# Kernel tuning notes

Measured on AMD Instinct MI355X. Metric: run time of the kernel, lower is better.

Reference implementation:

```python
import jax, jax.numpy as jnp
import numpy as np

D_MODEL = 1024
NUM_HEADS = 16
D_K = D_MODEL // NUM_HEADS


def setup_inputs() -> dict:
    key = jax.random.key(0)
    ks = jax.random.split(key, 11)
    B, S = 2, 2048
    scale = 1.0 / np.sqrt(D_MODEL)
    inp = {
        "v": jax.random.normal(ks[0], (B, S, D_MODEL), jnp.float32),
        "k": jax.random.normal(ks[1], (B, S, D_MODEL), jnp.float32),
        "q": jax.random.normal(ks[2], (B, S, D_MODEL), jnp.float32),
        "Wv": jax.random.normal(ks[3], (D_MODEL, D_MODEL), jnp.float32) * scale,
        "bv": jax.random.normal(ks[4], (D_MODEL,), jnp.float32) * 0.01,
        "Wk": jax.random.normal(ks[5], (D_MODEL, D_MODEL), jnp.float32) * scale,
        "bk": jax.random.normal(ks[6], (D_MODEL,), jnp.float32) * 0.01,
        "Wq": jax.random.normal(ks[7], (D_MODEL, D_MODEL), jnp.float32) * scale,
        "bq": jax.random.normal(ks[8], (D_MODEL,), jnp.float32) * 0.01,
        "Wo": jax.random.normal(ks[9], (D_MODEL, D_MODEL), jnp.float32) * scale,
        "bo": jax.random.normal(ks[10], (D_MODEL,), jnp.float32) * 0.01,
    }
    return inp


def reference(v, k, q, Wv, bv, Wk, bk, Wq, bq, Wo, bo):
    B, S, _ = q.shape
    # Linear projections (torch Linear: x @ W.T + b)
    vp = v @ Wv.T + bv
    kp = k @ Wk.T + bk
    qp = q @ Wq.T + bq
    # Split heads: [B, S, H, Dk]
    vp = vp.reshape(B, S, NUM_HEADS, D_K)
    kp = kp.reshape(B, S, NUM_HEADS, D_K)
    qp = qp.reshape(B, S, NUM_HEADS, D_K)
    # Scores [B, H, S, S], scaled softmax attention
    scores = jnp.einsum("bqhd,bkhd->bhqk", qp, kp) / jnp.sqrt(jnp.float32(D_K)).astype(qp.dtype)
    attn = jax.nn.softmax(scores, axis=-1)
    out = jnp.einsum("bhqk,bkhd->bqhd", attn, vp)
    out = out.reshape(B, S, D_MODEL)
    return out @ Wo.T + bo
```

## Files before the change

### kernel.cpp

```cpp
#include <hip/hip_runtime.h>
#include <math.h>

#define D 1024
#define NH 16
#define DK 64
#define S_LEN 2048
#define QSCALE 0.18033688011112f

using short8 = __attribute__((ext_vector_type(8))) short;
using f32x4  = __attribute__((ext_vector_type(4))) float;

#define MFMA16(a, b, c) __builtin_amdgcn_mfma_f32_16x16x32_bf16((a), (b), (c), 0, 0, 0)
#define EXP2F(x) __builtin_amdgcn_exp2f(x)

__device__ inline unsigned short f2bf(float f) {
    union { float f; unsigned u; } v; v.f = f;
    unsigned r = v.u + 0x7fffu + ((v.u >> 16) & 1u);
    return (unsigned short)(r >> 16);
}

__device__ inline void gload16(const unsigned short* g, unsigned short* l) {
    __builtin_amdgcn_global_load_lds(
        (const __attribute__((address_space(1))) void*)g,
        (__attribute__((address_space(3))) void*)l, 16, 0, 0);
}

struct CvtP {
    const float* s[7];
    unsigned short* d[7];
};
__global__ __launch_bounds__(256) void cvt_all(CvtP p, int inpBlocks, int wBlocks) {
    int bx = blockIdx.x;
    int seg, boff;
    if (bx < 3 * inpBlocks) { seg = bx / inpBlocks; boff = bx - seg * inpBlocks; }
    else { int t = bx - 3 * inpBlocks; seg = 3 + t / wBlocks; boff = t - (seg - 3) * wBlocks; }
    int i = (boff * 256 + threadIdx.x) * 4;
    float4 f = *(const float4*)(p.s[seg] + i);
    ushort4 u;
    u.x = f2bf(f.x); u.y = f2bf(f.y); u.z = f2bf(f.z); u.w = f2bf(f.w);
    *(ushort4*)(p.d[seg] + i) = u;
}


__global__ __launch_bounds__(256) void gemm_qkv(
    const unsigned short* __restrict__ qb, const unsigned short* __restrict__ kb,
    const unsigned short* __restrict__ vb,
    const unsigned short* __restrict__ Wqb, const unsigned short* __restrict__ Wkb,
    const unsigned short* __restrict__ Wvb,
    const float* __restrict__ bq, const float* __restrict__ bk, const float* __restrict__ bv,
    unsigned short* __restrict__ Qs, unsigned short* __restrict__ Ks,
    unsigned short* __restrict__ Vs)
{
    __shared__ unsigned short sA[128 * 32];
    __shared__ unsigned short sB[128 * 32];

    const int z = blockIdx.z;
    const unsigned short* X = (z == 0) ? qb : (z == 1) ? kb : vb;
    const unsigned short* W = (z == 0) ? Wqb : (z == 1) ? Wkb : Wvb;
    const float* bias = (z == 0) ? bq : (z == 1) ? bk : bv;

    const int tid = threadIdx.x, lane = tid & 63, w = tid >> 6;
    const int wy = w & 1, wx = w >> 1, r = lane & 15, q = lane >> 4;
    const int m0 = blockIdx.x * 128, n0 = blockIdx.y * 128;
    const int lrow = tid >> 2, lkc = (tid & 3) * 8;

    const unsigned short* Xg = X + (size_t)(m0 + lrow) * D + lkc;
    const unsigned short* Wg = W + (size_t)(n0 + lrow) * D + lkc;

    f32x4 acc[4][4];
    #pragma unroll
    for (int mi = 0; mi < 4; ++mi)
        #pragma unroll
        for (int ni = 0; ni < 4; ++ni) acc[mi][ni] = (f32x4){0.f, 0.f, 0.f, 0.f};

    for (int k0 = 0; k0 < D; k0 += 32) {
        __syncthreads();
        gload16(Xg + k0,          sA + w * 512);
        gload16(Xg + 64 * D + k0, sA + 2048 + w * 512);
        gload16(Wg + k0,          sB + w * 512);
        gload16(Wg + 64 * D + k0, sB + 2048 + w * 512);
        __syncthreads();
        short8 af[4], bfr[4];
        #pragma unroll
        for (int mi = 0; mi < 4; ++mi)
            af[mi] = *(const short8*)(sA + (wy * 64 + mi * 16 + r) * 32 + q * 8);
        #pragma unroll
        for (int ni = 0; ni < 4; ++ni)
            bfr[ni] = *(const short8*)(sB + (wx * 64 + ni * 16 + r) * 32 + q * 8);
        #pragma unroll
        for (int mi = 0; mi < 4; ++mi)
            #pragma unroll
            for (int ni = 0; ni < 4; ++ni)
                acc[mi][ni] = MFMA16(af[mi], bfr[ni], acc[mi][ni]);
    }

    float bcol[4];
    #pragma unroll
    for (int ni = 0; ni < 4; ++ni) bcol[ni] = bias[n0 + wx * 64 + ni * 16 + r];

    #pragma unroll
    for (int mi = 0; mi < 4; ++mi)
        #pragma unroll
        for (int ni = 0; ni < 4; ++ni)
            #pragma unroll
            for (int reg = 0; reg < 4; ++reg) {
                int row = m0 + wy * 64 + mi * 16 + q * 4 + reg;
                int col = n0 + wx * 64 + ni * 16 + r;
                float val = acc[mi][ni][reg] + bcol[ni];
                int bb = row >> 11, s = row & (S_LEN - 1);
                int hh = col >> 6, d = col & 63;
                if (z == 2) {
                    size_t off = (((size_t)bb * NH + hh) * 32 + (s >> 6)) * 4096
                               + (d >> 4) * 1024 + ((s & 63) >> 5) * 512
                               + (((s & 31) >> 3) * 16 + (d & 15)) * 8 + (s & 7);
                    Vs[off] = f2bf(val);
                } else {
                    size_t off = (((size_t)bb * NH + hh) * 128 + (s >> 4)) * 1024
                               + (d >> 5) * 512
                               + (((d & 31) >> 3) * 16 + (s & 15)) * 8 + (d & 7);
                    if (z == 0) Qs[off] = f2bf(val * QSCALE);
                    else        Ks[off] = f2bf(val);
                }
            }
}

__global__ __launch_bounds__(256) void gemm_o(
    const unsigned short* __restrict__ X, const unsigned short* __restrict__ W,
    const float* __restrict__ bias, float* __restrict__ out)
{
    __shared__ unsigned short sA[128 * 32];
    __shared__ unsigned short sB[64 * 32];

    const int tid = threadIdx.x, lane = tid & 63, w = tid >> 6;
    const int wy = w & 1, wx = w >> 1, r = lane & 15, q = lane >> 4;
    const int m0 = blockIdx.x * 128, n0 = blockIdx.y * 64;
    const int lrow = tid >> 2, lkc = (tid & 3) * 8;

    const unsigned short* Xg = X + (size_t)(m0 + lrow) * D + lkc;
    const unsigned short* Wg = W + (size_t)(n0 + lrow) * D + lkc;

    f32x4 acc[4][2];
    #pragma unroll
    for (int mi = 0; mi < 4; ++mi)
        #pragma unroll
        for (int ni = 0; ni < 2; ++ni) acc[mi][ni] = (f32x4){0.f, 0.f, 0.f, 0.f};

    for (int k0 = 0; k0 < D; k0 += 32) {
        __syncthreads();
        gload16(Xg + k0,          sA + w * 512);
        gload16(Xg + 64 * D + k0, sA + 2048 + w * 512);
        gload16(Wg + k0,          sB + w * 512);
        __syncthreads();
        short8 af[4], bfr[2];
        #pragma unroll
        for (int mi = 0; mi < 4; ++mi)
            af[mi] = *(const short8*)(sA + (wy * 64 + mi * 16 + r) * 32 + q * 8);
        #pragma unroll
        for (int ni = 0; ni < 2; ++ni)
            bfr[ni] = *(const short8*)(sB + (wx * 32 + ni * 16 + r) * 32 + q * 8);
        #pragma unroll
        for (int mi = 0; mi < 4; ++mi)
            #pragma unroll
            for (int ni = 0; ni < 2; ++ni)
                acc[mi][ni] = MFMA16(af[mi], bfr[ni], acc[mi][ni]);
    }

    float bcol[2];
    #pragma unroll
    for (int ni = 0; ni < 2; ++ni) bcol[ni] = bias[n0 + wx * 32 + ni * 16 + r];

    #pragma unroll
    for (int mi = 0; mi < 4; ++mi)
        #pragma unroll
        for (int ni = 0; ni < 2; ++ni)
            #pragma unroll
            for (int reg = 0; reg < 4; ++reg) {
                int row = m0 + wy * 64 + mi * 16 + q * 4 + reg;
                int col = n0 + wx * 32 + ni * 16 + r;
                out[(size_t)row * D + col] = acc[mi][ni][reg] + bcol[ni];
            }
}

__device__ __attribute__((always_inline)) inline void load_kfrag(
    const unsigned short* __restrict__ Kb, int blk16, int lane, short8 (&kf)[4][2])
{
    #pragma unroll
    for (int j = 0; j < 4; ++j)
        #pragma unroll
        for (int c = 0; c < 2; ++c)
            kf[j][c] = *(const short8*)(Kb + (size_t)(blk16 + j) * 1024 + c * 512 + lane * 8);
}

__device__ __attribute__((always_inline)) inline void attn_step(
    const unsigned short* __restrict__ Vb, int kvt, int lane, int r, int q,
    const short8 (&qf)[2][2], const short8 (&kf)[4][2],
    f32x4 (&O)[2][4], float (&psum)[2][4], unsigned short* __restrict__ sPw)
{
    short8 vf[4][2];
    #pragma unroll
    for (int nb = 0; nb < 4; ++nb)
        #pragma unroll
        for (int p = 0; p < 2; ++p)
            vf[nb][p] = *(const short8*)(Vb + (size_t)kvt * 4096 + nb * 1024 + p * 512 + lane * 8);

    f32x4 sc[2][4];
    #pragma unroll
    for (int j = 0; j < 4; ++j)
        #pragma unroll
        for (int rb = 0; rb < 2; ++rb) {
            f32x4 t = (f32x4){0.f, 0.f, 0.f, 0.f};
            t = MFMA16(qf[rb][0], kf[j][0], t);
            t = MFMA16(qf[rb][1], kf[j][1], t);
            sc[rb][j] = t;
        }

    #pragma unroll
    for (int rb = 0; rb < 2; ++rb)
        #pragma unroll
        for (int reg = 0; reg < 4; ++reg) {
            float p0 = EXP2F(sc[rb][0][reg]);
            float p1 = EXP2F(sc[rb][1][reg]);
            float p2 = EXP2F(sc[rb][2][reg]);
            float p3 = EXP2F(sc[rb][3][reg]);
            psum[rb][reg] += (p0 + p1) + (p2 + p3);
            int row = rb * 16 + q * 4 + reg;
            sPw[row * 72 + r]      = f2bf(p0);
            sPw[row * 72 + 16 + r] = f2bf(p1);
            sPw[row * 72 + 32 + r] = f2bf(p2);
            sPw[row * 72 + 48 + r] = f2bf(p3);
        }

    short8 pf[2][2];
    #pragma unroll
    for (int rb = 0; rb < 2; ++rb) {
        pf[rb][0] = *(const short8*)(sPw + (rb * 16 + r) * 72 + q * 8);
        pf[rb][1] = *(const short8*)(sPw + (rb * 16 + r) * 72 + 32 + q * 8);
    }

    #pragma unroll
    for (int nb = 0; nb < 4; ++nb)
        #pragma unroll
        for (int rb = 0; rb < 2; ++rb) {
            O[rb][nb] = MFMA16(pf[rb][0], vf[nb][0], O[rb][nb]);
            O[rb][nb] = MFMA16(pf[rb][1], vf[nb][1], O[rb][nb]);
        }
}

__global__ __launch_bounds__(256, 2) void attn_bf16(
    const unsigned short* __restrict__ Qs, const unsigned short* __restrict__ Ks,
    const unsigned short* __restrict__ Vs, unsigned short* __restrict__ AO)
{
    __shared__ unsigned short sP[4][32 * 72];

    const int tid = threadIdx.x, lane = tid & 63, w = tid >> 6;
    const int r = lane & 15, q = lane >> 4;
    const int q0 = blockIdx.x * 128;
    const int h = blockIdx.y, b = blockIdx.z;
    const int S = S_LEN;

    const unsigned short* Qb = Qs + ((size_t)b * NH + h) * 131072;
    const unsigned short* Kb = Ks + ((size_t)b * NH + h) * 131072;
    const unsigned short* Vb = Vs + ((size_t)b * NH + h) * 131072;
    unsigned short* sPw = sP[w];

    short8 qf[2][2];
    #pragma unroll
    for (int rb = 0; rb < 2; ++rb)
        #pragma unroll
        for (int c = 0; c < 2; ++c)
            qf[rb][c] = *(const short8*)(Qb + (size_t)((q0 >> 4) + 2 * w + rb) * 1024
                                            + c * 512 + lane * 8);

    f32x4 O[2][4];
    float psum[2][4];
    #pragma unroll
    for (int rb = 0; rb < 2; ++rb)
        #pragma unroll
        for (int i = 0; i < 4; ++i) { O[rb][i] = (f32x4){0.f, 0.f, 0.f, 0.f}; psum[rb][i] = 0.f; }

    short8 kfA[4][2], kfB[4][2];
    load_kfrag(Kb, 0, lane, kfA);

    for (int kvt = 0; kvt < 32; kvt += 2) {
        int n1 = (kvt + 1 < 32) ? (kvt + 1) * 4 : 124;
        load_kfrag(Kb, n1, lane, kfB);
        attn_step(Vb, kvt, lane, r, q, qf, kfA, O, psum, sPw);
        int n2 = (kvt + 2 < 32) ? (kvt + 2) * 4 : 124;
        load_kfrag(Kb, n2, lane, kfA);
        attn_step(Vb, kvt + 1, lane, r, q, qf, kfB, O, psum, sPw);
    }

    float inv[2][4];
    #pragma unroll
    for (int rb = 0; rb < 2; ++rb)
        #pragma unroll
        for (int reg = 0; reg < 4; ++reg) {
            float l = psum[rb][reg];
            #pragma unroll
            for (int off = 8; off > 0; off >>= 1) l += __shfl_xor(l, off);
            inv[rb][reg] = 1.0f / l;
        }

    unsigned short* Ob = AO + ((size_t)b * S + q0 + 32 * w) * D + h * DK;
    #pragma unroll
    for (int rb = 0; rb < 2; ++rb)
        #pragma unroll
        for (int reg = 0; reg < 4; ++reg)
            #pragma unroll
            for (int nb = 0; nb < 4; ++nb)
                Ob[(size_t)(rb * 16 + q * 4 + reg) * D + nb * 16 + r] =
                    f2bf(O[rb][nb][reg] * inv[rb][reg]);
}

extern "C" void kernel_launch(void* const* d_in, const int* in_sizes, int n_in,
                              void* d_out, int out_size, void* d_ws, size_t ws_size,
                              hipStream_t stream)
{
    const float* v  = (const float*)d_in[0];
    const float* k  = (const float*)d_in[1];
    const float* q  = (const float*)d_in[2];
    const float* Wv = (const float*)d_in[3];
    const float* bv = (const float*)d_in[4];
    const float* Wk = (const float*)d_in[5];
    const float* bk = (const float*)d_in[6];
    const float* Wq = (const float*)d_in[7];
    const float* bq = (const float*)d_in[8];
    const float* Wo = (const float*)d_in[9];
    const float* bo = (const float*)d_in[10];
    float* out = (float*)d_out;

    const int BS = in_sizes[0] / D;
    const int S  = S_LEN;
    const int B  = BS / S;

    char* ws = (char*)d_ws;
    unsigned short* qb  = (unsigned short*)(ws);
    unsigned short* kb  = (unsigned short*)(ws + 8388608);
    unsigned short* vb  = (unsigned short*)(ws + 16777216);
    unsigned short* Wqb = (unsigned short*)(ws + 25165824);
    unsigned short* Wkb = (unsigned short*)(ws + 27262976);
    unsigned short* Wvb = (unsigned short*)(ws + 29360128);
    unsigned short* Wob = (unsigned short*)(ws + 31457280);
    unsigned short* Qs  = (unsigned short*)(ws + 33554432);
    unsigned short* Ks  = (unsigned short*)(ws + 41943040);
    unsigned short* Vs  = (unsigned short*)(ws + 50331648);
    unsigned short* AO  = qb;

    dim3 blk(256);
    const int nInp = BS * D, nW = D * D;
    const int inpBlocks = nInp / 1024, wBlocks = nW / 1024;

    CvtP cp;
    cp.s[0] = q;  cp.d[0] = qb;
    cp.s[1] = k;  cp.d[1] = kb;
    cp.s[2] = v;  cp.d[2] = vb;
    cp.s[3] = Wq; cp.d[3] = Wqb;
    cp.s[4] = Wk; cp.d[4] = Wkb;
    cp.s[5] = Wv; cp.d[5] = Wvb;
    cp.s[6] = Wo; cp.d[6] = Wob;
    cvt_all<<<3 * inpBlocks + 4 * wBlocks, blk, 0, stream>>>(cp, inpBlocks, wBlocks);

    dim3 qkvgrid(BS / 128, D / 128, 3);
    gemm_qkv<<<qkvgrid, blk, 0, stream>>>(qb, kb, vb, Wqb, Wkb, Wvb,
                                          bq, bk, bv, Qs, Ks, Vs);

    dim3 agrid(S / 128, NH, B);
    attn_bf16<<<agrid, blk, 0, stream>>>(Qs, Ks, Vs, AO);

    dim3 ogrid(BS / 128, D / 64);
    gemm_o<<<ogrid, blk, 0, stream>>>(AO, Wob, bo, out);
}
```

Measured before the change: 222.2 us.

## Double GEMM K-tile to 64 and permute V layout for packed P stores

Both projection GEMMs now stage 64-wide K slices per iteration, halving the barrier and loop count, at the cost of doubling shared memory per block. In attention, the kv index order of V is permuted so each lane's four probabilities can go to shared memory as one packed 8-byte store instead of four scalar stores. The V permutation must stay consistent with the P column ordering. The larger LDS footprint may reduce occupancy.

New measurement: 280.7 us. 26.4% more time.

```diff
diff --git a/kernel.cpp b/kernel.cpp
--- a/kernel.cpp
+++ b/kernel.cpp
@@ -51,8 +51,8 @@
     unsigned short* __restrict__ Qs, unsigned short* __restrict__ Ks,
     unsigned short* __restrict__ Vs)
 {
-    __shared__ unsigned short sA[128 * 32];
-    __shared__ unsigned short sB[128 * 32];
+    __shared__ unsigned short sA[128 * 64];
+    __shared__ unsigned short sB[128 * 64];
 
     const int z = blockIdx.z;
     const unsigned short* X = (z == 0) ? qb : (z == 1) ? kb : vb;
@@ -62,7 +62,7 @@
     const int tid = threadIdx.x, lane = tid & 63, w = tid >> 6;
     const int wy = w & 1, wx = w >> 1, r = lane & 15, q = lane >> 4;
     const int m0 = blockIdx.x * 128, n0 = blockIdx.y * 128;
-    const int lrow = tid >> 2, lkc = (tid & 3) * 8;
+    const int lrow = tid >> 3, lkc = (tid & 7) * 8;
 
     const unsigned short* Xg = X + (size_t)(m0 + lrow) * D + lkc;
     const unsigned short* Wg = W + (size_t)(n0 + lrow) * D + lkc;
@@ -73,25 +73,32 @@
         #pragma unroll
         for (int ni = 0; ni < 4; ++ni) acc[mi][ni] = (f32x4){0.f, 0.f, 0.f, 0.f};
 
-    for (int k0 = 0; k0 < D; k0 += 32) {
+    for (int k0 = 0; k0 < D; k0 += 64) {
         __syncthreads();
         gload16(Xg + k0,          sA + w * 512);
-        gload16(Xg + 64 * D + k0, sA + 2048 + w * 512);
+        gload16(Xg + 32 * D + k0, sA + 2048 + w * 512);
+        gload16(Xg + 64 * D + k0, sA + 4096 + w * 512);
+        gload16(Xg + 96 * D + k0, sA + 6144 + w * 512);
         gload16(Wg + k0,          sB + w * 512);
-        gload16(Wg + 64 * D + k0, sB + 2048 + w * 512);
+        gload16(Wg + 32 * D + k0, sB + 2048 + w * 512);
+        gload16(Wg + 64 * D + k0, sB + 4096 + w * 512);
+        gload16(Wg + 96 * D + k0, sB + 6144 + w * 512);
         __syncthreads();
-        short8 af[4], bfr[4];
-        #pragma unroll
-        for (int mi = 0; mi < 4; ++mi)
-            af[mi] = *(const short8*)(sA + (wy * 64 + mi * 16 + r) * 32 + q * 8);
-        #pragma unroll
-        for (int ni = 0; ni < 4; ++ni)
-            bfr[ni] = *(const short8*)(sB + (wx * 64 + ni * 16 + r) * 32 + q * 8);
-        #pragma unroll
-        for (int mi = 0; mi < 4; ++mi)
+        #pragma unroll
+        for (int c = 0; c < 2; ++c) {
+            short8 af[4], bfr[4];
+            #pragma unroll
+            for (int mi = 0; mi < 4; ++mi)
+                af[mi] = *(const short8*)(sA + (wy * 64 + mi * 16 + r) * 64 + c * 32 + q * 8);
             #pragma unroll
             for (int ni = 0; ni < 4; ++ni)
-                acc[mi][ni] = MFMA16(af[mi], bfr[ni], acc[mi][ni]);
+                bfr[ni] = *(const short8*)(sB + (wx * 64 + ni * 16 + r) * 64 + c * 32 + q * 8);
+            #pragma unroll
+            for (int mi = 0; mi < 4; ++mi)
+                #pragma unroll
+                for (int ni = 0; ni < 4; ++ni)
+                    acc[mi][ni] = MFMA16(af[mi], bfr[ni], acc[mi][ni]);
+        }
     }
 
     float bcol[4];
@@ -110,9 +117,11 @@
                 int bb = row >> 11, s = row & (S_LEN - 1);
                 int hh = col >> 6, d = col & 63;
                 if (z == 2) {
+                    int kv = s & 63;
+                    int kvp = ((kv & 15) << 2) | (kv >> 4);
                     size_t off = (((size_t)bb * NH + hh) * 32 + (s >> 6)) * 4096
-                               + (d >> 4) * 1024 + ((s & 63) >> 5) * 512
-                               + (((s & 31) >> 3) * 16 + (d & 15)) * 8 + (s & 7);
+                               + (d >> 4) * 1024 + (kvp >> 5) * 512
+                               + (((kvp & 31) >> 3) * 16 + (d & 15)) * 8 + (kvp & 7);
                     Vs[off] = f2bf(val);
                 } else {
                     size_t off = (((size_t)bb * NH + hh) * 128 + (s >> 4)) * 1024
@@ -128,13 +137,13 @@
     const unsigned short* __restrict__ X, const unsigned short* __restrict__ W,
     const float* __restrict__ bias, float* __restrict__ out)
 {
-    __shared__ unsigned short sA[128 * 32];
-    __shared__ unsigned short sB[64 * 32];
+    __shared__ unsigned short sA[128 * 64];
+    __shared__ unsigned short sB[64 * 64];
 
     const int tid = threadIdx.x, lane = tid & 63, w = tid >> 6;
     const int wy = w & 1, wx = w >> 1, r = lane & 15, q = lane >> 4;
     const int m0 = blockIdx.x * 128, n0 = blockIdx.y * 64;
-    const int lrow = tid >> 2, lkc = (tid & 3) * 8;
+    const int lrow = tid >> 3, lkc = (tid & 7) * 8;
 
     const unsigned short* Xg = X + (size_t)(m0 + lrow) * D + lkc;
     const unsigned short* Wg = W + (size_t)(n0 + lrow) * D + lkc;
@@ -145,24 +154,30 @@
         #pragma unroll
         for (int ni = 0; ni < 2; ++ni) acc[mi][ni] = (f32x4){0.f, 0.f, 0.f, 0.f};
 
-    for (int k0 = 0; k0 < D; k0 += 32) {
+    for (int k0 = 0; k0 < D; k0 += 64) {
         __syncthreads();
         gload16(Xg + k0,          sA + w * 512);
-        gload16(Xg + 64 * D + k0, sA + 2048 + w * 512);
+        gload16(Xg + 32 * D + k0, sA + 2048 + w * 512);
+        gload16(Xg + 64 * D + k0, sA + 4096 + w * 512);
+        gload16(Xg + 96 * D + k0, sA + 6144 + w * 512);
         gload16(Wg + k0,          sB + w * 512);
+        gload16(Wg + 32 * D + k0, sB + 2048 + w * 512);
         __syncthreads();
-        short8 af[4], bfr[2];
-        #pragma unroll
-        for (int mi = 0; mi < 4; ++mi)
-            af[mi] = *(const short8*)(sA + (wy * 64 + mi * 16 + r) * 32 + q * 8);
-        #pragma unroll
-        for (int ni = 0; ni < 2; ++ni)
-            bfr[ni] = *(const short8*)(sB + (wx * 32 + ni * 16 + r) * 32 + q * 8);
-        #pragma unroll
-        for (int mi = 0; mi < 4; ++mi)
+        #pragma unroll
+        for (int c = 0; c < 2; ++c) {
+            short8 af[4], bfr[2];
+            #pragma unroll
+            for (int mi = 0; mi < 4; ++mi)
+                af[mi] = *(const short8*)(sA + (wy * 64 + mi * 16 + r) * 64 + c * 32 + q * 8);
             #pragma unroll
             for (int ni = 0; ni < 2; ++ni)
-                acc[mi][ni] = MFMA16(af[mi], bfr[ni], acc[mi][ni]);
+                bfr[ni] = *(const short8*)(sB + (wx * 32 + ni * 16 + r) * 64 + c * 32 + q * 8);
+            #pragma unroll
+            for (int mi = 0; mi < 4; ++mi)
+                #pragma unroll
+                for (int ni = 0; ni < 2; ++ni)
+                    acc[mi][ni] = MFMA16(af[mi], bfr[ni], acc[mi][ni]);
+        }
     }
 
     float bcol[2];
@@ -224,10 +239,9 @@
             float p3 = EXP2F(sc[rb][3][reg]);
             psum[rb][reg] += (p0 + p1) + (p2 + p3);
             int row = rb * 16 + q * 4 + reg;
-            sPw[row * 72 + r]      = f2bf(p0);
-            sPw[row * 72 + 16 + r] = f2bf(p1);
-            sPw[row * 72 + 32 + r] = f2bf(p2);
-            sPw[row * 72 + 48 + r] = f2bf(p3);
+            ushort4 pk;
+            pk.x = f2bf(p0); pk.y = f2bf(p1); pk.z = f2bf(p2); pk.w = f2bf(p3);
+            *(ushort4*)(sPw + row * 72 + 4 * r) = pk;
         }
 
     short8 pf[2][2];
```

## Stage QKV epilogue through LDS and make O-proj read MFMA-swizzled operands directly

Applied to the files above, without the earlier changes.

The QKV GEMM epilogue now writes bias-added bf16 tiles into shared memory in the attention-ready swizzled layout, then copies them out as coalesced 16-byte stores instead of scattered 2-byte stores. Attention writes its output in a fragment-swizzled layout through LDS, and Wo gets its own swizzling conversion kernel. This lets the output-projection GEMM load MFMA fragments straight from global memory with register double-buffering and no LDS or barriers. Batch and sequence sizes are now hardcoded, and the O GEMM relies on cache hits with no shared-memory reuse.

Result: slower. 237.3 us (+6.8%).

```diff
diff --git a/kernel.cpp b/kernel.cpp
--- a/kernel.cpp
+++ b/kernel.cpp
@@ -26,8 +26,8 @@
 }
 
 struct CvtP {
-    const float* s[7];
-    unsigned short* d[7];
+    const float* s[6];
+    unsigned short* d[6];
 };
 __global__ __launch_bounds__(256) void cvt_all(CvtP p, int inpBlocks, int wBlocks) {
     int bx = blockIdx.x;
@@ -41,6 +41,22 @@
     *(ushort4*)(p.d[seg] + i) = u;
 }
 
+__global__ __launch_bounds__(256) void wo_swz(const float* __restrict__ Wo,
+                                              unsigned short* __restrict__ Wos) {
+    const int t = threadIdx.x, lane = t & 63;
+    const int r = lane & 15, j = (lane >> 4) & 3;
+    const int nblk = blockIdx.x;
+    const int p = blockIdx.y * 4 + (t >> 6);
+    const int n = nblk * 16 + r;
+    const int k = p * 32 + j * 8;
+    float4 f0 = *(const float4*)(Wo + (size_t)n * D + k);
+    float4 f1 = *(const float4*)(Wo + (size_t)n * D + k + 4);
+    short8 o;
+    o[0] = f2bf(f0.x); o[1] = f2bf(f0.y); o[2] = f2bf(f0.z); o[3] = f2bf(f0.w);
+    o[4] = f2bf(f1.x); o[5] = f2bf(f1.y); o[6] = f2bf(f1.z); o[7] = f2bf(f1.w);
+    *(short8*)(Wos + (size_t)nblk * 16384 + p * 512 + lane * 8) = o;
+}
+
 
 __global__ __launch_bounds__(256) void gemm_qkv(
     const unsigned short* __restrict__ qb, const unsigned short* __restrict__ kb,
@@ -51,8 +67,9 @@
     unsigned short* __restrict__ Qs, unsigned short* __restrict__ Ks,
     unsigned short* __restrict__ Vs)
 {
-    __shared__ unsigned short sA[128 * 32];
-    __shared__ unsigned short sB[128 * 32];
+    __shared__ unsigned short smem[16384];
+    unsigned short* sA = smem;
+    unsigned short* sB = smem + 4096;
 
     const int z = blockIdx.z;
     const unsigned short* X = (z == 0) ? qb : (z == 1) ? kb : vb;
@@ -98,46 +115,71 @@
     #pragma unroll
     for (int ni = 0; ni < 4; ++ni) bcol[ni] = bias[n0 + wx * 64 + ni * 16 + r];
 
-    #pragma unroll
-    for (int mi = 0; mi < 4; ++mi)
-        #pragma unroll
-        for (int ni = 0; ni < 4; ++ni)
-            #pragma unroll
-            for (int reg = 0; reg < 4; ++reg) {
-                int row = m0 + wy * 64 + mi * 16 + q * 4 + reg;
-                int col = n0 + wx * 64 + ni * 16 + r;
-                float val = acc[mi][ni][reg] + bcol[ni];
-                int bb = row >> 11, s = row & (S_LEN - 1);
-                int hh = col >> 6, d = col & 63;
-                if (z == 2) {
-                    size_t off = (((size_t)bb * NH + hh) * 32 + (s >> 6)) * 4096
-                               + (d >> 4) * 1024 + ((s & 63) >> 5) * 512
-                               + (((s & 31) >> 3) * 16 + (d & 15)) * 8 + (s & 7);
-                    Vs[off] = f2bf(val);
-                } else {
-                    size_t off = (((size_t)bb * NH + hh) * 128 + (s >> 4)) * 1024
-                               + (d >> 5) * 512
-                               + (((d & 31) >> 3) * 16 + (s & 15)) * 8 + (d & 7);
-                    if (z == 0) Qs[off] = f2bf(val * QSCALE);
-                    else        Ks[off] = f2bf(val);
+    const int bb = m0 >> 11;
+    const int sBase = m0 & (S_LEN - 1);
+    const int hh0 = n0 >> 6;
+
+    __syncthreads();
+
+    if (z != 2) {
+        const float sc = (z == 0) ? QSCALE : 1.0f;
+        #pragma unroll
+        for (int mi = 0; mi < 4; ++mi)
+            #pragma unroll
+            for (int ni = 0; ni < 4; ++ni)
+                #pragma unroll
+                for (int reg = 0; reg < 4; ++reg) {
+                    float val = (acc[mi][ni][reg] + bcol[ni]) * sc;
+                    int off = (wx * 8 + wy * 4 + mi) * 1024 + (ni >> 1) * 512
+                            + (((ni & 1) * 2 + (r >> 3)) * 16 + q * 4 + reg) * 8 + (r & 7);
+                    smem[off] = f2bf(val);
                 }
-            }
-}
-
-__global__ __launch_bounds__(256) void gemm_o(
-    const unsigned short* __restrict__ X, const unsigned short* __restrict__ W,
+        __syncthreads();
+        unsigned short* dst = (z == 0) ? Qs : Ks;
+        #pragma unroll
+        for (int kk = 0; kk < 8; ++kk) {
+            int idx = tid + 256 * kk;
+            int ci = idx >> 7, within = idx & 127;
+            int hh_l = ci >> 3, sblk_l = ci & 7;
+            size_t g = ((size_t)bb * NH + hh0 + hh_l) * 131072
+                     + (size_t)((sBase >> 4) + sblk_l) * 1024 + within * 8;
+            *(short8*)(dst + g) = *(const short8*)(smem + idx * 8);
+        }
+    } else {
+        #pragma unroll
+        for (int mi = 0; mi < 4; ++mi)
+            #pragma unroll
+            for (int ni = 0; ni < 4; ++ni)
+                #pragma unroll
+                for (int reg = 0; reg < 4; ++reg) {
+                    float val = acc[mi][ni][reg] + bcol[ni];
+                    int off = (wx * 2 + wy) * 4096 + ni * 1024 + (mi >> 1) * 512
+                            + (((mi & 1) * 2 + (q >> 1)) * 16 + r) * 8 + (q & 1) * 4 + reg;
+                    smem[off] = f2bf(val);
+                }
+        __syncthreads();
+        #pragma unroll
+        for (int kk = 0; kk < 8; ++kk) {
+            int idx = tid + 256 * kk;
+            int ci = idx >> 9, within = idx & 511;
+            int hh_l = ci >> 1, vt_l = ci & 1;
+            size_t g = ((size_t)bb * NH + hh0 + hh_l) * 131072
+                     + (size_t)((sBase >> 6) + vt_l) * 4096 + within * 8;
+            *(short8*)(Vs + g) = *(const short8*)(smem + idx * 8);
+        }
+    }
+}
+
+__global__ __launch_bounds__(256, 2) void gemm_o(
+    const unsigned short* __restrict__ AO, const unsigned short* __restrict__ Wos,
     const float* __restrict__ bias, float* __restrict__ out)
 {
-    __shared__ unsigned short sA[128 * 32];
-    __shared__ unsigned short sB[64 * 32];
-
     const int tid = threadIdx.x, lane = tid & 63, w = tid >> 6;
     const int wy = w & 1, wx = w >> 1, r = lane & 15, q = lane >> 4;
     const int m0 = blockIdx.x * 128, n0 = blockIdx.y * 64;
-    const int lrow = tid >> 2, lkc = (tid & 3) * 8;
-
-    const unsigned short* Xg = X + (size_t)(m0 + lrow) * D + lkc;
-    const unsigned short* Wg = W + (size_t)(n0 + lrow) * D + lkc;
+
+    const unsigned short* Ab = AO + (size_t)((m0 >> 4) + wy * 4) * 16384 + lane * 8;
+    const unsigned short* Bb = Wos + (size_t)((n0 >> 4) + wx * 2) * 16384 + lane * 8;
 
     f32x4 acc[4][2];
     #pragma unroll
@@ -145,24 +187,33 @@
         #pragma unroll
         for (int ni = 0; ni < 2; ++ni) acc[mi][ni] = (f32x4){0.f, 0.f, 0.f, 0.f};
 
-    for (int k0 = 0; k0 < D; k0 += 32) {
-        __syncthreads();
-        gload16(Xg + k0,          sA + w * 512);
-        gload16(Xg + 64 * D + k0, sA + 2048 + w * 512);
-        gload16(Wg + k0,          sB + w * 512);
-        __syncthreads();
-        short8 af[4], bfr[2];
-        #pragma unroll
-        for (int mi = 0; mi < 4; ++mi)
-            af[mi] = *(const short8*)(sA + (wy * 64 + mi * 16 + r) * 32 + q * 8);
-        #pragma unroll
-        for (int ni = 0; ni < 2; ++ni)
-            bfr[ni] = *(const short8*)(sB + (wx * 32 + ni * 16 + r) * 32 + q * 8);
+    short8 afA[4], bfA[2], afB[4], bfB[2];
+    #pragma unroll
+    for (int mi = 0; mi < 4; ++mi) afA[mi] = *(const short8*)(Ab + (size_t)mi * 16384);
+    #pragma unroll
+    for (int ni = 0; ni < 2; ++ni) bfA[ni] = *(const short8*)(Bb + (size_t)ni * 16384);
+
+    for (int p = 0; p < 32; p += 2) {
+        int p1 = (p + 1 < 32) ? p + 1 : 31;
+        #pragma unroll
+        for (int mi = 0; mi < 4; ++mi) afB[mi] = *(const short8*)(Ab + (size_t)mi * 16384 + p1 * 512);
+        #pragma unroll
+        for (int ni = 0; ni < 2; ++ni) bfB[ni] = *(const short8*)(Bb + (size_t)ni * 16384 + p1 * 512);
         #pragma unroll
         for (int mi = 0; mi < 4; ++mi)
             #pragma unroll
             for (int ni = 0; ni < 2; ++ni)
-                acc[mi][ni] = MFMA16(af[mi], bfr[ni], acc[mi][ni]);
+                acc[mi][ni] = MFMA16(afA[mi], bfA[ni], acc[mi][ni]);
+        int p2 = (p + 2 < 32) ? p + 2 : 31;
+        #pragma unroll
+        for (int mi = 0; mi < 4; ++mi) afA[mi] = *(const short8*)(Ab + (size_t)mi * 16384 + p2 * 512);
+        #pragma unroll
+        for (int ni = 0; ni < 2; ++ni) bfA[ni] = *(const short8*)(Bb + (size_t)ni * 16384 + p2 * 512);
+        #pragma unroll
+        for (int mi = 0; mi < 4; ++mi)
+            #pragma unroll
+            for (int ni = 0; ni < 2; ++ni)
+                acc[mi][ni] = MFMA16(afB[mi], bfB[ni], acc[mi][ni]);
     }
 
     float bcol[2];
@@ -256,7 +307,6 @@
     const int r = lane & 15, q = lane >> 4;
     const int q0 = blockIdx.x * 128;
     const int h = blockIdx.y, b = blockIdx.z;
-    const int S = S_LEN;
 
     const unsigned short* Qb = Qs + ((size_t)b * NH + h) * 131072;
     const unsigned short* Kb = Ks + ((size_t)b * NH + h) * 131072;
@@ -301,15 +351,25 @@
             inv[rb][reg] = 1.0f / l;
         }
 
-    unsigned short* Ob = AO + ((size_t)b * S + q0 + 32 * w) * D + h * DK;
     #pragma unroll
     for (int rb = 0; rb < 2; ++rb)
         #pragma unroll
         for (int reg = 0; reg < 4; ++reg)
             #pragma unroll
-            for (int nb = 0; nb < 4; ++nb)
-                Ob[(size_t)(rb * 16 + q * 4 + reg) * D + nb * 16 + r] =
-                    f2bf(O[rb][nb][reg] * inv[rb][reg]);
+            for (int nb = 0; nb < 4; ++nb) {
+                int ld = nb * 16 + r;
+                int off = (rb * 2 + (nb >> 1)) * 512
+                        + (((nb & 1) * 2 + (r >> 3)) * 16 + q * 4 + reg) * 8 + (r & 7);
+                sPw[off] = f2bf(O[rb][nb][reg] * inv[rb][reg]);
+                (void)ld;
+            }
+    #pragma unroll
+    for (int kk = 0; kk < 4; ++kk) {
+        int rb = kk >> 1, panel = kk & 1;
+        size_t g = (size_t)(b * 128 + (q0 >> 4) + 2 * w + rb) * 16384
+                 + (size_t)(h * 2 + panel) * 512 + lane * 8;
+        *(short8*)(AO + g) = *(const short8*)(sPw + kk * 512 + lane * 8);
+    }
 }
 
 extern "C" void kernel_launch(void* const* d_in, const int* in_sizes, int n_in,
@@ -330,8 +390,7 @@
     float* out = (float*)d_out;
 
     const int BS = in_sizes[0] / D;
-    const int S  = S_LEN;
-    const int B  = BS / S;
+    (void)BS;
 
     char* ws = (char*)d_ws;
     unsigned short* qb  = (unsigned short*)(ws);
@@ -340,14 +399,14 @@
     unsigned short* Wqb = (unsigned short*)(ws + 25165824);
     unsigned short* Wkb = (unsigned short*)(ws + 27262976);
     unsigned short* Wvb = (unsigned short*)(ws + 29360128);
-    unsigned short* Wob = (unsigned short*)(ws + 31457280);
+    unsigned short* Wos = (unsigned short*)(ws + 31457280);
     unsigned short* Qs  = (unsigned short*)(ws + 33554432);
     unsigned short* Ks  = (unsigned short*)(ws + 41943040);
     unsigned short* Vs  = (unsigned short*)(ws + 50331648);
     unsigned short* AO  = qb;
 
     dim3 blk(256);
-    const int nInp = BS * D, nW = D * D;
+    const int nInp = 4096 * D, nW = D * D;
     const int inpBlocks = nInp / 1024, wBlocks = nW / 1024;
 
     CvtP cp;
@@ -357,16 +416,18 @@
     cp.s[3] = Wq; cp.d[3] = Wqb;
     cp.s[4] = Wk; cp.d[4] = Wkb;
     cp.s[5] = Wv; cp.d[5] = Wvb;
-    cp.s[6] = Wo; cp.d[6] = Wob;
-    cvt_all<<<3 * inpBlocks + 4 * wBlocks, blk, 0, stream>>>(cp, inpBlocks, wBlocks);
-
-    dim3 qkvgrid(BS / 128, D / 128, 3);
+    cvt_all<<<3 * inpBlocks + 3 * wBlocks, blk, 0, stream>>>(cp, inpBlocks, wBlocks);
+
+    dim3 wgrid(64, 8);
+    wo_swz<<<wgrid, blk, 0, stream>>>(Wo, Wos);
+
+    dim3 qkvgrid(4096 / 128, D / 128, 3);
     gemm_qkv<<<qkvgrid, blk, 0, stream>>>(qb, kb, vb, Wqb, Wkb, Wvb,
                                           bq, bk, bv, Qs, Ks, Vs);
 
-    dim3 agrid(S / 128, NH, B);
+    dim3 agrid(S_LEN / 128, NH, 2);
     attn_bf16<<<agrid, blk, 0, stream>>>(Qs, Ks, Vs, AO);
 
-    dim3 ogrid(BS / 128, D / 64);
-    gemm_o<<<ogrid, blk, 0, stream>>>(AO, Wob, bo, out);
-}
+    dim3 ogrid(4096 / 128, D / 64);
+    gemm_o<<<ogrid, blk, 0, stream>>>(AO, Wos, bo, out);
+}
```
